# Optimization experiments

Hardware: AMD Instinct MI355X
Metric: run time of the kernel (lower is better)

The kernel has to match this reference:

```python
import jax, jax.numpy as jnp
import numpy as np

B, T, C = 2, 2048, 2048
NH, NKVH = 16, 4
HS = C // NH  # 128
NEG_INF = -1e30


def _rope_freqs(T, hs, base=10000.0):
    inv = 1.0 / (base ** (np.arange(0, hs, 2, dtype=np.float32) / hs))  # [hs/2]
    ang = np.arange(T, dtype=np.float32)[:, None] * inv[None, :]        # [T, hs/2]
    return jnp.asarray(np.cos(ang)), jnp.asarray(np.sin(ang))


def setup_inputs() -> dict:
    key = jax.random.key(0)
    ks = jax.random.split(key, 4)
    x = jax.random.normal(ks[0], (B, T, C), dtype=jnp.float32)
    W_attn = jax.random.normal(ks[1], (C, C + 2 * NKVH * HS), dtype=jnp.float32) * 0.02
    b_attn = jnp.zeros((C + 2 * NKVH * HS,), dtype=jnp.float32)
    W_proj = jax.random.normal(ks[2], (C, C), dtype=jnp.float32) * 0.02
    b_proj = jnp.zeros((C,), dtype=jnp.float32)
    freqs_cos, freqs_sin = _rope_freqs(T, HS)
    return {"x": x, "freqs_cos": freqs_cos, "freqs_sin": freqs_sin,
            "W_attn": W_attn, "b_attn": b_attn, "W_proj": W_proj, "b_proj": b_proj}


def _apply_rope(x, cos, sin):
    # x: [B, T, H, hs]; cos/sin: [T, hs/2] -> broadcast [1, T, 1, hs/2]
    b, t, h, hs = x.shape
    x_ = x.reshape(b, t, h, hs // 2, 2)
    re, im = x_[..., 0], x_[..., 1]
    c = cos[None, :, None, :]
    s = sin[None, :, None, :]
    out_re = re * c - im * s
    out_im = re * s + im * c
    return jnp.stack([out_re, out_im], axis=-1).reshape(b, t, h, hs)


def reference(x, freqs_cos, freqs_sin, W_attn, b_attn, W_proj, b_proj):
    b, t, c = x.shape
    qkv = x @ W_attn + b_attn                                   # [B,T,C+2*nkvh*hs]
    q, k, v = jnp.split(qkv, [c, c + NKVH * HS], axis=2)
    q = q.reshape(b, t, NH, HS)
    k = k.reshape(b, t, NKVH, HS)
    v = v.reshape(b, t, NKVH, HS)
    q = _apply_rope(q, freqs_cos, freqs_sin)
    k = _apply_rope(k, freqs_cos, freqs_sin)
    # group heads: q [B, nkvh, rep, T, hs]; k,v [B, nkvh, T, hs]
    rep = NH // NKVH
    q = q.transpose(0, 2, 1, 3).reshape(b, NKVH, rep, t, HS)
    k = k.transpose(0, 2, 1, 3)
    v = v.transpose(0, 2, 1, 3)
    scale = 1.0 / jnp.sqrt(jnp.asarray(HS, dtype=x.dtype))
    scores = jnp.einsum('bgrth,bgsh->bgrts', q, k) * scale      # [B,g,rep,T,T]
    causal = jnp.tril(jnp.ones((t, t), dtype=bool))
    scores = jnp.where(causal[None, None, None], scores, NEG_INF)
    att = jax.nn.softmax(scores, axis=-1)
    y = jnp.einsum('bgrts,bgsh->bgrth', att, v)                 # [B,g,rep,T,hs]
    y = y.reshape(b, NH, t, HS).transpose(0, 2, 1, 3).reshape(b, t, c)
    return y @ W_proj + b_proj
```

## Files before the change

### kernel.cpp

```cpp
#include <hip/hip_runtime.h>
#include <hip/hip_bf16.h>
#include <stdint.h>

#define B_ 2
#define T_ 2048
#define C_ 2048
#define NH_ 16
#define NKVH_ 4
#define HS_ 128
#define QKV_ 3072
#define NTOK_ 4096

typedef __attribute__((ext_vector_type(4))) float f32x4;
typedef __attribute__((ext_vector_type(8))) short s16x8;

__device__ __forceinline__ short f2bf(float f) {
    union { float f; unsigned u; } v; v.f = f;
    unsigned r = v.u + 0x7FFFu + ((v.u >> 16) & 1u);
    return (short)(r >> 16);
}

__device__ __forceinline__ void async16(const void* g, void* l) {
    __builtin_amdgcn_global_load_lds(
        (const __attribute__((address_space(1))) void*)g,
        (__attribute__((address_space(3))) void*)l, 16, 0, 0);
}

__global__ void cast_bf16_kernel(const float* __restrict__ x, short* __restrict__ out, int n8) {
    int i = blockIdx.x * 256 + threadIdx.x;
    if (i >= n8) return;
    const float4* p = (const float4*)x + (size_t)i * 2;
    float4 a = p[0], b = p[1];
    short o[8] = { f2bf(a.x), f2bf(a.y), f2bf(a.z), f2bf(a.w),
                   f2bf(b.x), f2bf(b.y), f2bf(b.z), f2bf(b.w) };
    *(int4*)(out + (size_t)i * 8) = *(const int4*)o;
}

__global__ void transcast(const float* __restrict__ W, short* __restrict__ WT, int Kd, int Nd) {
    __shared__ float tile[64][65];
    int k0 = blockIdx.x * 64, n0 = blockIdx.y * 64;
    int tid = threadIdx.x;
    int cl = tid & 63, rw = tid >> 6;
    for (int it = 0; it < 16; ++it) {
        int r = it * 4 + rw;
        tile[r][cl] = W[(size_t)(k0 + r) * Nd + n0 + cl];
    }
    __syncthreads();
    for (int it = 0; it < 16; ++it) {
        int n = it * 4 + rw;
        WT[(size_t)(n0 + n) * Kd + k0 + cl] = f2bf(tile[cl][n]);
    }
}

__global__ __launch_bounds__(256, 2) void gemm_bt(
    const short* __restrict__ A, const short* __restrict__ Bt,
    const float* __restrict__ bias, float* __restrict__ Cc,
    int M, int N, int K)
{
    __shared__ short As[128 * 64];
    __shared__ short Bs[128 * 64];
    int tid = threadIdx.x;
    int w = tid >> 6, l = tid & 63;
    int lr = l & 15, lg = l >> 4;
    int bm = blockIdx.x, bn = blockIdx.y;
    int wm = (w >> 1) * 64, wn = (w & 1) * 64;
    f32x4 acc[4][4];
#pragma unroll
    for (int i = 0; i < 4; i++)
#pragma unroll
        for (int j = 0; j < 4; j++) { acc[i][j][0]=0.f; acc[i][j][1]=0.f; acc[i][j][2]=0.f; acc[i][j][3]=0.f; }
    int arow = l >> 3, acol = (l & 7) * 8;
    for (int k0 = 0; k0 < K; k0 += 64) {
#pragma unroll
        for (int i = 0; i < 4; i++) {
            int chunk = w * 4 + i;
            int row = chunk * 8 + arow;
            async16(A  + (size_t)(bm * 128 + row) * K + k0 + acol, (char*)As + chunk * 1024);
            async16(Bt + (size_t)(bn * 128 + row) * K + k0 + acol, (char*)Bs + chunk * 1024);
        }
        __syncthreads();
#pragma unroll
        for (int ks = 0; ks < 2; ks++) {
            s16x8 af[4], bf[4];
#pragma unroll
            for (int mi = 0; mi < 4; mi++)
                af[mi] = *(const s16x8*)&As[(wm + mi * 16 + lr) * 64 + ks * 32 + lg * 8];
#pragma unroll
            for (int ni = 0; ni < 4; ni++)
                bf[ni] = *(const s16x8*)&Bs[(wn + ni * 16 + lr) * 64 + ks * 32 + lg * 8];
#pragma unroll
            for (int mi = 0; mi < 4; mi++)
#pragma unroll
                for (int ni = 0; ni < 4; ni++)
                    acc[mi][ni] = __builtin_amdgcn_mfma_f32_16x16x32_bf16(af[mi], bf[ni], acc[mi][ni], 0, 0, 0);
        }
        __syncthreads();
    }
#pragma unroll
    for (int mi = 0; mi < 4; mi++) {
        int row = bm * 128 + wm + mi * 16 + lg * 4;
#pragma unroll
        for (int ni = 0; ni < 4; ni++) {
            int col = bn * 128 + wn + ni * 16 + lr;
            float bv = bias[col];
#pragma unroll
            for (int j = 0; j < 4; j++)
                Cc[(size_t)(row + j) * N + col] = acc[mi][ni][j] + bv;
        }
    }
}

__global__ void rope_scatter(const float* __restrict__ qkv,
                             const float* __restrict__ fcos, const float* __restrict__ fsin,
                             short* __restrict__ Q, short* __restrict__ Kb)
{
    const float qscale = 0.08838834764831845f;
    int idx = blockIdx.x * 256 + threadIdx.x;
    int tok = idx / 1280, p = idx - tok * 1280;
    if (tok >= NTOK_) return;
    int b = tok >> 11, t = tok & 2047;
    if (p < 1024) {
        int h = p >> 6, i = p & 63;
        const float* src = qkv + (size_t)tok * QKV_ + h * 128 + 2 * i;
        float re = src[0], im = src[1];
        float c = fcos[t * 64 + i], s = fsin[t * 64 + i];
        unsigned lo = (unsigned short)f2bf((re * c - im * s) * qscale);
        unsigned hi = (unsigned short)f2bf((re * s + im * c) * qscale);
        *(unsigned*)(Q + ((size_t)(b * NH_ + h) * T_ + t) * HS_ + 2 * i) = lo | (hi << 16);
    } else {
        int pk = p - 1024; int g = pk >> 6, i = pk & 63;
        const float* src = qkv + (size_t)tok * QKV_ + C_ + g * 128 + 2 * i;
        float re = src[0], im = src[1];
        float c = fcos[t * 64 + i], s = fsin[t * 64 + i];
        unsigned lo = (unsigned short)f2bf(re * c - im * s);
        unsigned hi = (unsigned short)f2bf(re * s + im * c);
        *(unsigned*)(Kb + ((size_t)(b * NKVH_ + g) * T_ + t) * HS_ + 2 * i) = lo | (hi << 16);
    }
}

__global__ void v_transpose(const float* __restrict__ qkv, short* __restrict__ VT) {
    __shared__ float tile[64][65];
    int t0 = blockIdx.x * 64, d0 = blockIdx.y * 64;
    int bg = blockIdx.z; int b = bg >> 2, g = bg & 3;
    int tid = threadIdx.x; int cl = tid & 63, rw = tid >> 6;
    const float* base = qkv + (size_t)(b * T_ + t0) * QKV_ + C_ + NKVH_ * HS_ + g * HS_ + d0;
    for (int it = 0; it < 16; ++it) {
        int r = it * 4 + rw;
        tile[r][cl] = base[(size_t)r * QKV_ + cl];
    }
    __syncthreads();
    short* out = VT + ((size_t)(b * NKVH_ + g) * HS_ + d0) * T_ + t0;
    for (int it = 0; it < 16; ++it) {
        int d = it * 4 + rw;
        out[(size_t)d * T_ + cl] = f2bf(tile[cl][d]);
    }
}

__global__ __launch_bounds__(256, 2) void attn_kernel(
    const short* __restrict__ Qg, const short* __restrict__ Kg,
    const short* __restrict__ VTg, short* __restrict__ Y)
{
    __shared__ short Ks[2][64 * 128];
    __shared__ short VTs[2][128 * 64];
    __shared__ short Ps[4][16 * 64];
    int tid = threadIdx.x, w = tid >> 6, l = tid & 63;
    int lr = l & 15, lg = l >> 4;
    int qt = 31 - (int)blockIdx.y;
    int bh = blockIdx.x;
    int b = bh >> 4, h = bh & 15, g = h >> 2;
    const short* Qb = Qg + (size_t)(b * NH_ + h) * T_ * HS_;
    const short* Kb = Kg + (size_t)(b * NKVH_ + g) * T_ * HS_;
    const short* Vb = VTg + (size_t)(b * NKVH_ + g) * HS_ * T_;

    auto STAGE = [&](int st, int buf) {
#pragma unroll
        for (int i = 0; i < 4; i++) {
            int chunk = w * 4 + i;
            int poff = chunk * 1024 + l * 16;
            int qoffk = poff ^ (((poff >> 8) & 7) << 4);
            async16(Kb + (size_t)(st * 64 + (qoffk >> 8)) * HS_ + ((qoffk & 255) >> 1),
                    (char*)&Ks[buf][0] + chunk * 1024);
            int qoffv = poff ^ (((poff >> 7) & 7) << 4);
            async16(Vb + (size_t)(qoffv >> 7) * T_ + st * 64 + ((qoffv & 127) >> 1),
                    (char*)&VTs[buf][0] + chunk * 1024);
        }
    };

    s16x8 qf[4];
    int qrow = qt * 64 + w * 16 + lr;
#pragma unroll
    for (int kc = 0; kc < 4; kc++)
        qf[kc] = *(const s16x8*)(Qb + (size_t)qrow * HS_ + kc * 32 + lg * 8);

    f32x4 oacc[8];
#pragma unroll
    for (int i = 0; i < 8; i++) { oacc[i][0]=0.f; oacc[i][1]=0.f; oacc[i][2]=0.f; oacc[i][3]=0.f; }
    float m[4] = {-1e30f, -1e30f, -1e30f, -1e30f};
    float lsum[4] = {0.f, 0.f, 0.f, 0.f};
    int qg0 = qt * 64 + w * 16 + lg * 4;

    STAGE(0, 0);
    __syncthreads();
    int cur = 0;

    for (int st = 0; st <= qt; ++st) {
        if (st < qt) STAGE(st + 1, cur ^ 1);
        const char* KsC = (const char*)&Ks[cur][0];
        const char* VsC = (const char*)&VTs[cur][0];

        f32x4 sv[4];
#pragma unroll
        for (int ni = 0; ni < 4; ni++) {
            f32x4 a; a[0]=0.f; a[1]=0.f; a[2]=0.f; a[3]=0.f;
#pragma unroll
            for (int kc = 0; kc < 4; kc++) {
                int lo = ((ni * 16 + lr) << 8) + ((kc * 32 + lg * 8) << 1);
                int po = lo ^ (((lo >> 8) & 7) << 4);
                s16x8 kf = *(const s16x8*)(KsC + po);
                a = __builtin_amdgcn_mfma_f32_16x16x32_bf16(qf[kc], kf, a, 0, 0, 0);
            }
            sv[ni] = a;
        }
        float tmax[4] = {-1e30f, -1e30f, -1e30f, -1e30f};
        if (st == qt) {
#pragma unroll
            for (int ni = 0; ni < 4; ni++) {
                int sg = st * 64 + ni * 16 + lr;
#pragma unroll
                for (int j = 0; j < 4; j++) {
                    float s = sv[ni][j];
                    if (sg > qg0 + j) s = -1e30f;
                    sv[ni][j] = s;
                    tmax[j] = fmaxf(tmax[j], s);
                }
            }
        } else {
#pragma unroll
            for (int ni = 0; ni < 4; ni++)
#pragma unroll
                for (int j = 0; j < 4; j++)
                    tmax[j] = fmaxf(tmax[j], sv[ni][j]);
        }
#pragma unroll
        for (int msk = 1; msk < 16; msk <<= 1)
#pragma unroll
            for (int j = 0; j < 4; j++)
                tmax[j] = fmaxf(tmax[j], __shfl_xor(tmax[j], msk));
        bool need = (tmax[0] > m[0]) | (tmax[1] > m[1]) | (tmax[2] > m[2]) | (tmax[3] > m[3]);
        if (__any(need)) {
#pragma unroll
            for (int j = 0; j < 4; j++) {
                float mn = fmaxf(m[j], tmax[j]);
                float corr = __expf(m[j] - mn);
                m[j] = mn;
                lsum[j] *= corr;
#pragma unroll
                for (int dn = 0; dn < 8; dn++) oacc[dn][j] *= corr;
            }
        }
#pragma unroll
        for (int ni = 0; ni < 4; ni++)
#pragma unroll
            for (int j = 0; j < 4; j++) {
                float p = __expf(sv[ni][j] - m[j]);
                sv[ni][j] = p;
                lsum[j] += p;
            }
#pragma unroll
        for (int ni = 0; ni < 4; ni++)
#pragma unroll
            for (int j = 0; j < 4; j++) {
                int lo = (lg * 4 + j) * 128 + (ni * 16 + lr) * 2;
                int po = lo ^ (((lo >> 7) & 7) << 4);
                *(short*)((char*)&Ps[w][0] + po) = f2bf(sv[ni][j]);
            }
#pragma unroll
        for (int sc = 0; sc < 2; sc++) {
            int lo = lr * 128 + sc * 64 + lg * 16;
            int po = lo ^ (((lo >> 7) & 7) << 4);
            s16x8 pf = *(const s16x8*)((const char*)&Ps[w][0] + po);
#pragma unroll
            for (int dn = 0; dn < 8; dn++) {
                int lov = (dn * 16 + lr) * 128 + (sc * 32 + lg * 8) * 2;
                int pov = lov ^ (((lov >> 7) & 7) << 4);
                s16x8 vf = *(const s16x8*)(VsC + pov);
                oacc[dn] = __builtin_amdgcn_mfma_f32_16x16x32_bf16(pf, vf, oacc[dn], 0, 0, 0);
            }
        }
        __syncthreads();
        cur ^= 1;
    }

#pragma unroll
    for (int msk = 1; msk < 16; msk <<= 1)
#pragma unroll
        for (int j = 0; j < 4; j++)
            lsum[j] += __shfl_xor(lsum[j], msk);
    float inv[4];
#pragma unroll
    for (int j = 0; j < 4; j++) inv[j] = 1.0f / lsum[j];
#pragma unroll
    for (int dn = 0; dn < 8; dn++)
#pragma unroll
        for (int j = 0; j < 4; j++) {
            int trow = qt * 64 + w * 16 + lg * 4 + j;
            Y[(size_t)(b * T_ + trow) * C_ + h * 128 + dn * 16 + lr] = f2bf(oacc[dn][j] * inv[j]);
        }
}

extern "C" void kernel_launch(void* const* d_in, const int* in_sizes, int n_in,
                              void* d_out, int out_size, void* d_ws, size_t ws_size,
                              hipStream_t stream)
{
    const float* x      = (const float*)d_in[0];
    const float* fcos   = (const float*)d_in[1];
    const float* fsin   = (const float*)d_in[2];
    const float* W_attn = (const float*)d_in[3];
    const float* b_attn = (const float*)d_in[4];
    const float* W_proj = (const float*)d_in[5];
    const float* b_proj = (const float*)d_in[6];
    float* out = (float*)d_out;
    char* ws = (char*)d_ws;

    short* xb  = (short*)(ws + 0);
    float* qkv = (float*)(ws + 16777216);
    short* y   = (short*)(ws + 16777216);
    short* WpT = (short*)(ws + 33554432);
    short* WaT = (short*)(ws + 67108864);
    short* Qb  = (short*)(ws + 67108864);
    short* Kb  = (short*)(ws + 83886080);
    short* VT  = (short*)(ws + 88080384);

    cast_bf16_kernel<<<4096, 256, 0, stream>>>(x, xb, NTOK_ * C_ / 8);
    transcast<<<dim3(32, 48), 256, 0, stream>>>(W_attn, WaT, C_, QKV_);
    gemm_bt<<<dim3(32, 24), 256, 0, stream>>>(xb, WaT, b_attn, qkv, NTOK_, QKV_, C_);
    rope_scatter<<<20480, 256, 0, stream>>>(qkv, fcos, fsin, Qb, Kb);
    v_transpose<<<dim3(32, 2, 8), 256, 0, stream>>>(qkv, VT);
    transcast<<<dim3(32, 32), 256, 0, stream>>>(W_proj, WpT, C_, C_);
    attn_kernel<<<dim3(32, 32), 256, 0, stream>>>(Qb, Kb, VT, y);
    gemm_bt<<<dim3(32, 16), 256, 0, stream>>>(y, WpT, b_proj, out, NTOK_, C_, C_);
}
```

Before: 230.5 us.

## Use 32x32x16 MFMA with 128-row query tiles in attention kernel

The attention kernel now gives each block 128 query rows (32 per wave) instead of 64, and uses 32x32x16 bf16 MFMAs with transposed operand roles, so each lane owns one query row. Each K/V tile loaded into LDS is reused by twice as many queries, and the softmax row reductions need fewer shuffles. Output stores are packed into pairs. The cost is half as many blocks (512), more causal imbalance within a block, waves idling on stages past their diagonal, and higher register pressure.

```diff
diff --git a/kernel.cpp b/kernel.cpp
--- a/kernel.cpp
+++ b/kernel.cpp
@@ -12,6 +12,7 @@
 #define NTOK_ 4096
 
 typedef __attribute__((ext_vector_type(4))) float f32x4;
+typedef __attribute__((ext_vector_type(16))) float f32x16;
 typedef __attribute__((ext_vector_type(8))) short s16x8;
 
 __device__ __forceinline__ short f2bf(float f) {
@@ -162,10 +163,10 @@
 {
     __shared__ short Ks[2][64 * 128];
     __shared__ short VTs[2][128 * 64];
-    __shared__ short Ps[4][16 * 64];
+    __shared__ short Ps[4][32 * 64];
     int tid = threadIdx.x, w = tid >> 6, l = tid & 63;
-    int lr = l & 15, lg = l >> 4;
-    int qt = 31 - (int)blockIdx.y;
+    int l31 = l & 31, hi = l >> 5;
+    int qt = 15 - (int)blockIdx.y;
     int bh = blockIdx.x;
     int b = bh >> 4, h = bh & 15, g = h >> 2;
     const short* Qb = Qg + (size_t)(b * NH_ + h) * T_ * HS_;
@@ -186,125 +187,112 @@
         }
     };
 
-    s16x8 qf[4];
-    int qrow = qt * 64 + w * 16 + lr;
-#pragma unroll
-    for (int kc = 0; kc < 4; kc++)
-        qf[kc] = *(const s16x8*)(Qb + (size_t)qrow * HS_ + kc * 32 + lg * 8);
-
-    f32x4 oacc[8];
-#pragma unroll
-    for (int i = 0; i < 8; i++) { oacc[i][0]=0.f; oacc[i][1]=0.f; oacc[i][2]=0.f; oacc[i][3]=0.f; }
-    float m[4] = {-1e30f, -1e30f, -1e30f, -1e30f};
-    float lsum[4] = {0.f, 0.f, 0.f, 0.f};
-    int qg0 = qt * 64 + w * 16 + lg * 4;
+    int qw = qt * 128 + w * 32;
+    int qglob = qw + l31;
+
+    s16x8 qf[8];
+#pragma unroll
+    for (int dc = 0; dc < 8; dc++)
+        qf[dc] = *(const s16x8*)(Qb + (size_t)qglob * HS_ + dc * 16 + hi * 8);
+
+    f32x16 oacc[4];
+#pragma unroll
+    for (int db = 0; db < 4; db++)
+#pragma unroll
+        for (int i = 0; i < 16; i++) oacc[db][i] = 0.f;
+    float m = -1e30f, lsum = 0.f;
+    int nst = 2 * qt + 2;
 
     STAGE(0, 0);
     __syncthreads();
     int cur = 0;
 
-    for (int st = 0; st <= qt; ++st) {
-        if (st < qt) STAGE(st + 1, cur ^ 1);
-        const char* KsC = (const char*)&Ks[cur][0];
-        const char* VsC = (const char*)&VTs[cur][0];
-
-        f32x4 sv[4];
-#pragma unroll
-        for (int ni = 0; ni < 4; ni++) {
-            f32x4 a; a[0]=0.f; a[1]=0.f; a[2]=0.f; a[3]=0.f;
-#pragma unroll
-            for (int kc = 0; kc < 4; kc++) {
-                int lo = ((ni * 16 + lr) << 8) + ((kc * 32 + lg * 8) << 1);
-                int po = lo ^ (((lo >> 8) & 7) << 4);
-                s16x8 kf = *(const s16x8*)(KsC + po);
-                a = __builtin_amdgcn_mfma_f32_16x16x32_bf16(qf[kc], kf, a, 0, 0, 0);
+    for (int st = 0; st < nst; ++st) {
+        if (st + 1 < nst) STAGE(st + 1, cur ^ 1);
+        if (st * 64 <= qw) {
+            const char* KsC = (const char*)&Ks[cur][0];
+            const char* VsC = (const char*)&VTs[cur][0];
+            char* PsC = (char*)&Ps[w][0];
+
+            f32x16 sacc[2];
+#pragma unroll
+            for (int sb = 0; sb < 2; sb++) {
+                f32x16 a;
+#pragma unroll
+                for (int i = 0; i < 16; i++) a[i] = 0.f;
+#pragma unroll
+                for (int dc = 0; dc < 8; dc++) {
+                    int lo = (sb * 32 + l31) * 256 + dc * 32 + hi * 16;
+                    int po = lo ^ (((lo >> 8) & 7) << 4);
+                    s16x8 kf = *(const s16x8*)(KsC + po);
+                    a = __builtin_amdgcn_mfma_f32_32x32x16_bf16(kf, qf[dc], a, 0, 0, 0);
+                }
+                sacc[sb] = a;
             }
-            sv[ni] = a;
-        }
-        float tmax[4] = {-1e30f, -1e30f, -1e30f, -1e30f};
-        if (st == qt) {
-#pragma unroll
-            for (int ni = 0; ni < 4; ni++) {
-                int sg = st * 64 + ni * 16 + lr;
-#pragma unroll
-                for (int j = 0; j < 4; j++) {
-                    float s = sv[ni][j];
-                    if (sg > qg0 + j) s = -1e30f;
-                    sv[ni][j] = s;
-                    tmax[j] = fmaxf(tmax[j], s);
+            if (st * 64 + 63 > qw) {
+#pragma unroll
+                for (int sb = 0; sb < 2; sb++)
+#pragma unroll
+                    for (int r = 0; r < 16; r++) {
+                        int s = st * 64 + sb * 32 + (r & 3) + 8 * (r >> 2) + 4 * hi;
+                        if (s > qglob) sacc[sb][r] = -1e30f;
+                    }
+            }
+            float tm = -1e30f;
+#pragma unroll
+            for (int sb = 0; sb < 2; sb++)
+#pragma unroll
+                for (int r = 0; r < 16; r++) tm = fmaxf(tm, sacc[sb][r]);
+            tm = fmaxf(tm, __shfl_xor(tm, 32));
+            if (__any(tm > m)) {
+                float mn = fmaxf(m, tm);
+                float corr = __expf(m - mn);
+                m = mn; lsum *= corr;
+#pragma unroll
+                for (int db = 0; db < 4; db++)
+#pragma unroll
+                    for (int r = 0; r < 16; r++) oacc[db][r] *= corr;
+            }
+#pragma unroll
+            for (int sb = 0; sb < 2; sb++)
+#pragma unroll
+                for (int r = 0; r < 16; r++) {
+                    float p = __expf(sacc[sb][r] - m);
+                    lsum += p;
+                    int sl = sb * 32 + (r & 3) + 8 * (r >> 2) + 4 * hi;
+                    int lo = l31 * 128 + sl * 2;
+                    int po = lo ^ (((lo >> 7) & 7) << 4);
+                    *(short*)(PsC + po) = f2bf(p);
+                }
+#pragma unroll
+            for (int sc = 0; sc < 4; sc++) {
+                int lp = l31 * 128 + sc * 32 + hi * 16;
+                int pp = lp ^ (((lp >> 7) & 7) << 4);
+                s16x8 pf = *(const s16x8*)(PsC + pp);
+#pragma unroll
+                for (int db = 0; db < 4; db++) {
+                    int lo = (db * 32 + l31) * 128 + sc * 32 + hi * 16;
+                    int po = lo ^ (((lo >> 7) & 7) << 4);
+                    s16x8 vf = *(const s16x8*)(VsC + po);
+                    oacc[db] = __builtin_amdgcn_mfma_f32_32x32x16_bf16(vf, pf, oacc[db], 0, 0, 0);
                 }
             }
-        } else {
-#pragma unroll
-            for (int ni = 0; ni < 4; ni++)
-#pragma unroll
-                for (int j = 0; j < 4; j++)
-                    tmax[j] = fmaxf(tmax[j], sv[ni][j]);
-        }
-#pragma unroll
-        for (int msk = 1; msk < 16; msk <<= 1)
-#pragma unroll
-            for (int j = 0; j < 4; j++)
-                tmax[j] = fmaxf(tmax[j], __shfl_xor(tmax[j], msk));
-        bool need = (tmax[0] > m[0]) | (tmax[1] > m[1]) | (tmax[2] > m[2]) | (tmax[3] > m[3]);
-        if (__any(need)) {
-#pragma unroll
-            for (int j = 0; j < 4; j++) {
-                float mn = fmaxf(m[j], tmax[j]);
-                float corr = __expf(m[j] - mn);
-                m[j] = mn;
-                lsum[j] *= corr;
-#pragma unroll
-                for (int dn = 0; dn < 8; dn++) oacc[dn][j] *= corr;
-            }
-        }
-#pragma unroll
-        for (int ni = 0; ni < 4; ni++)
-#pragma unroll
-            for (int j = 0; j < 4; j++) {
-                float p = __expf(sv[ni][j] - m[j]);
-                sv[ni][j] = p;
-                lsum[j] += p;
-            }
-#pragma unroll
-        for (int ni = 0; ni < 4; ni++)
-#pragma unroll
-            for (int j = 0; j < 4; j++) {
-                int lo = (lg * 4 + j) * 128 + (ni * 16 + lr) * 2;
-                int po = lo ^ (((lo >> 7) & 7) << 4);
-                *(short*)((char*)&Ps[w][0] + po) = f2bf(sv[ni][j]);
-            }
-#pragma unroll
-        for (int sc = 0; sc < 2; sc++) {
-            int lo = lr * 128 + sc * 64 + lg * 16;
-            int po = lo ^ (((lo >> 7) & 7) << 4);
-            s16x8 pf = *(const s16x8*)((const char*)&Ps[w][0] + po);
-#pragma unroll
-            for (int dn = 0; dn < 8; dn++) {
-                int lov = (dn * 16 + lr) * 128 + (sc * 32 + lg * 8) * 2;
-                int pov = lov ^ (((lov >> 7) & 7) << 4);
-                s16x8 vf = *(const s16x8*)(VsC + pov);
-                oacc[dn] = __builtin_amdgcn_mfma_f32_16x16x32_bf16(pf, vf, oacc[dn], 0, 0, 0);
-            }
         }
         __syncthreads();
         cur ^= 1;
     }
 
-#pragma unroll
-    for (int msk = 1; msk < 16; msk <<= 1)
-#pragma unroll
-        for (int j = 0; j < 4; j++)
-            lsum[j] += __shfl_xor(lsum[j], msk);
-    float inv[4];
-#pragma unroll
-    for (int j = 0; j < 4; j++) inv[j] = 1.0f / lsum[j];
-#pragma unroll
-    for (int dn = 0; dn < 8; dn++)
-#pragma unroll
-        for (int j = 0; j < 4; j++) {
-            int trow = qt * 64 + w * 16 + lg * 4 + j;
-            Y[(size_t)(b * T_ + trow) * C_ + h * 128 + dn * 16 + lr] = f2bf(oacc[dn][j] * inv[j]);
+    lsum += __shfl_xor(lsum, 32);
+    float inv = 1.0f / lsum;
+    short* Yrow = Y + (size_t)(b * T_ + qglob) * C_ + h * 128;
+#pragma unroll
+    for (int db = 0; db < 4; db++)
+#pragma unroll
+        for (int pr = 0; pr < 8; pr++) {
+            unsigned u0 = (unsigned short)f2bf(oacc[db][2 * pr] * inv);
+            unsigned u1 = (unsigned short)f2bf(oacc[db][2 * pr + 1] * inv);
+            int d = db * 32 + ((2 * pr) & 3) + 8 * (pr >> 1) + 4 * hi;
+            *(unsigned*)(Yrow + d) = u0 | (u1 << 16);
         }
 }
 
@@ -337,6 +325,6 @@
     rope_scatter<<<20480, 256, 0, stream>>>(qkv, fcos, fsin, Qb, Kb);
     v_transpose<<<dim3(32, 2, 8), 256, 0, stream>>>(qkv, VT);
     transcast<<<dim3(32, 32), 256, 0, stream>>>(W_proj, WpT, C_, C_);
-    attn_kernel<<<dim3(32, 32), 256, 0, stream>>>(Qb, Kb, VT, y);
+    attn_kernel<<<dim3(32, 16), 256, 0, stream>>>(Qb, Kb, VT, y);
     gemm_bt<<<dim3(32, 16), 256, 0, stream>>>(y, WpT, b_proj, out, NTOK_, C_, C_);
 }
```

Result: faster. 225.3 us (-2.3%).
